# Optimization experiments

Measured on AMD Instinct MI355X. Metric: run time of the kernel, lower is better.

The kernel has to match this reference:

```python
import jax, jax.numpy as jnp
import numpy as np

DIM = 512
L = 64            # block_size == attn_block_size (pool=1)
H = 8             # num_heads
HD = DIM // H     # head_dim
KEY = L + 1       # leaf nodes + block node ('64x65' layout)


def setup_inputs() -> dict:
    key = jax.random.key(0)
    ks = jax.random.split(key, 8)
    B, N, C = 2, 32768, DIM
    nb = N // L
    x = jax.random.normal(ks[0], (B, N, C), dtype=jnp.float32)
    attn_mask = jax.random.randint(ks[1], (B, nb, L, KEY), 0, 2, dtype=jnp.int32)
    # ensure the block node is always attendable so no query row is fully masked
    attn_mask = attn_mask.at[:, :, :, L].set(1)
    edge_feats = jax.random.normal(ks[2], (B, nb, L, KEY, 4), dtype=jnp.float32)
    qkv_w = jax.random.normal(ks[3], (3 * C, C), dtype=jnp.float32) * 0.02
    qkv_b = jax.random.normal(ks[4], (3 * C,), dtype=jnp.float32) * 0.02
    proj_w = jax.random.normal(ks[5], (C, C), dtype=jnp.float32) * 0.02
    proj_b = jax.random.normal(ks[6], (C,), dtype=jnp.float32) * 0.02
    eg_w = jax.random.normal(ks[7], (H, 4), dtype=jnp.float32) * 0.01
    eg_b = jnp.zeros((H,), dtype=jnp.float32)
    return {"x": x, "attn_mask": attn_mask, "edge_feats": edge_feats,
            "qkv_w": qkv_w, "qkv_b": qkv_b, "proj_w": proj_w, "proj_b": proj_b,
            "eg_w": eg_w, "eg_b": eg_b}


def reference(x, attn_mask, edge_feats, qkv_w, qkv_b, proj_w, proj_b, eg_w, eg_b):
    B, N, C = x.shape
    nb = N // L
    scale = HD ** -0.5

    xb = x.reshape(B, nb, L, C)                         # queries = leaf nodes
    block_node = xb.mean(axis=2, keepdims=True)         # [B, nb, 1, C]
    kv = jnp.concatenate([xb, block_node], axis=2)      # [B, nb, KEY, C]

    q = xb @ qkv_w[:C].T + qkv_b[:C]
    k = kv @ qkv_w[C:2 * C].T + qkv_b[C:2 * C]
    v = kv @ qkv_w[2 * C:].T + qkv_b[2 * C:]

    q = q.reshape(B, nb, L, H, HD)
    k = k.reshape(B, nb, KEY, H, HD)
    v = v.reshape(B, nb, KEY, H, HD)

    scores = jnp.einsum('bnqhd,bnkhd->bnqkh', q, k) * scale

    # physics bias: zero special (block) node + diagonal, channel 3 forced to 1
    bias = edge_feats[..., :4]
    bias = bias.at[:, :, :, L, :].set(0.0).at[:, :, :, L, 3].set(1.0)
    idx = jnp.arange(L)
    bias = bias.at[:, :, idx, idx, :].set(0.0).at[:, :, idx, idx, 3].set(1.0)

    scores = scores + bias[..., 3:4]

    masked = (attn_mask == 0)[..., None]                # [B, nb, q, k, 1]
    scores = jnp.where(masked, -jnp.inf, scores)
    attn_probs = jax.nn.softmax(scores, axis=3)

    lew = bias @ eg_w.T + eg_b                          # [B, nb, q, k, H]
    lew = jnp.where(masked, 0.0, lew)
    combined = attn_probs + lew

    out = jnp.einsum('bnqkh,bnkhd->bnqhd', combined, v).reshape(B, nb, L, C)
    out = out @ proj_w.T + proj_b
    return out.reshape(B, N, C)
```

## Files before the change

### kernel.cpp

```cpp
#include <hip/hip_runtime.h>
#include <hip/hip_bf16.h>
#include <math.h>

constexpr int LQ   = 64;
constexpr int KEYS = 65;
constexpr int NH   = 8;
constexpr int DH   = 64;
constexpr int CC   = 512;
constexpr int TOK  = 65536;
constexpr int NBLK = 1024;
constexpr int MEXT = TOK + NBLK;
constexpr int QKVLD = 3 * CC;

using s16x8 = __attribute__((ext_vector_type(8))) short;
using f32x4 = __attribute__((ext_vector_type(4))) float;

__device__ __forceinline__ unsigned short f2bf(float f) {
  unsigned int u = __float_as_uint(f);
  u += 0x7fffu + ((u >> 16) & 1u);
  return (unsigned short)(u >> 16);
}

__global__ __launch_bounds__(256) void prep_x_kernel(const float* __restrict__ x,
                                                     unsigned short* __restrict__ xe) {
  const int blk = blockIdx.x;
  const int c = threadIdx.x * 2;
  const long base = (long)blk * LQ * CC;
  float s0 = 0.f, s1 = 0.f;
  for (int r = 0; r < LQ; ++r) {
    const float2 v = *(const float2*)(x + base + (long)r * CC + c);
    s0 += v.x; s1 += v.y;
    unsigned int p = (unsigned int)f2bf(v.x) | ((unsigned int)f2bf(v.y) << 16);
    *(unsigned int*)(xe + base + (long)r * CC + c) = p;
  }
  unsigned int pm = (unsigned int)f2bf(s0 * (1.f / 64.f)) |
                    ((unsigned int)f2bf(s1 * (1.f / 64.f)) << 16);
  *(unsigned int*)(xe + ((long)TOK + blk) * CC + c) = pm;
}

__global__ __launch_bounds__(256) void prep_w_kernel(const float* __restrict__ qkvw,
                                                     const float* __restrict__ projw,
                                                     unsigned short* __restrict__ wq,
                                                     unsigned short* __restrict__ wp) {
  const int i = blockIdx.x * 256 + threadIdx.x;
  const float* src; unsigned short* dst; int j;
  if (i < 196608) { src = qkvw; dst = wq; j = i; }
  else            { src = projw; dst = wp; j = i - 196608; }
  const float4 v = *(const float4*)(src + (long)j * 4);
  unsigned int lo = (unsigned int)f2bf(v.x) | ((unsigned int)f2bf(v.y) << 16);
  unsigned int hi = (unsigned int)f2bf(v.z) | ((unsigned int)f2bf(v.w) << 16);
  uint2 o; o.x = lo; o.y = hi;
  *(uint2*)(dst + (long)j * 4) = o;
}

template <bool OUT_F32>
__global__ __launch_bounds__(256) void gemm_bt_kernel(
    const unsigned short* __restrict__ A,
    const unsigned short* __restrict__ Bw,
    const float* __restrict__ bias,
    void* __restrict__ Cv,
    int M, int Nn, int K, int tilesN) {
  __shared__ unsigned short lA[128 * 32];
  __shared__ unsigned short lB[128 * 32];
  const int bm = blockIdx.x / tilesN;
  const int bn = blockIdx.x % tilesN;
  const int t = threadIdx.x;
  const int w = t >> 6, lane = t & 63;
  const int l15 = lane & 15, l4 = lane >> 4;
  const int wr = w >> 1, wc = w & 1;
  const int srow = lane >> 2;
  const int scol = (lane & 3) * 8;
  const long rowA0 = (long)bm * 128;
  const long rowB0 = (long)bn * 128;
  f32x4 acc[4][4] = {};
  for (int kk = 0; kk < K; kk += 32) {
#pragma unroll
    for (int i = 0; i < 2; ++i) {
      const int rc = w + 4 * i;
      const unsigned short* gA = A + (rowA0 + rc * 16 + srow) * K + kk + scol;
      const unsigned short* gB = Bw + (rowB0 + rc * 16 + srow) * K + kk + scol;
      __builtin_amdgcn_global_load_lds((const __attribute__((address_space(1))) void*)gA,
                                       (__attribute__((address_space(3))) void*)(lA + rc * 16 * 32),
                                       16, 0, 0);
      __builtin_amdgcn_global_load_lds((const __attribute__((address_space(1))) void*)gB,
                                       (__attribute__((address_space(3))) void*)(lB + rc * 16 * 32),
                                       16, 0, 0);
    }
    __syncthreads();
    s16x8 af[4], bfr[4];
#pragma unroll
    for (int m = 0; m < 4; ++m)
      af[m] = *(const s16x8*)(lA + (wr * 64 + m * 16 + l15) * 32 + l4 * 8);
#pragma unroll
    for (int n = 0; n < 4; ++n)
      bfr[n] = *(const s16x8*)(lB + (wc * 64 + n * 16 + l15) * 32 + l4 * 8);
#pragma unroll
    for (int m = 0; m < 4; ++m)
#pragma unroll
      for (int n = 0; n < 4; ++n)
        acc[m][n] = __builtin_amdgcn_mfma_f32_16x16x32_bf16(af[m], bfr[n], acc[m][n], 0, 0, 0);
    __syncthreads();
  }
#pragma unroll
  for (int m = 0; m < 4; ++m) {
    const long row0 = rowA0 + wr * 64 + m * 16 + l4 * 4;
#pragma unroll
    for (int n = 0; n < 4; ++n) {
      const int col = (int)rowB0 + wc * 64 + n * 16 + l15;
      const float bv = bias[col];
#pragma unroll
      for (int r = 0; r < 4; ++r) {
        const float v = acc[m][n][r] + bv;
        if (OUT_F32) ((float*)Cv)[(row0 + r) * (long)Nn + col] = v;
        else ((unsigned short*)Cv)[(row0 + r) * (long)Nn + col] = f2bf(v);
      }
    }
  }
}

__global__ __launch_bounds__(512) void attn_kernel(
    const unsigned short* __restrict__ QKV,
    const int* __restrict__ amask,
    const float* __restrict__ edge,
    const float* __restrict__ egw,
    const float* __restrict__ egb,
    unsigned short* __restrict__ AO) {
  __shared__ unsigned short PS[NH][16 * 104];
  const int blk = blockIdx.x;
  const int t = threadIdx.x;
  const int h = t >> 6, lane = t & 63;
  const int l15 = lane & 15, l4 = lane >> 4;
  const long tokb = (long)blk * LQ;
  const long bnrow = (long)TOK + blk;
  const unsigned short* Qb = QKV + h * DH;
  const unsigned short* Kb = QKV + CC + h * DH;
  const unsigned short* Vb = QKV + 2 * CC + h * DH;
  const float eg0 = egw[h * 4 + 0], eg1 = egw[h * 4 + 1];
  const float eg2 = egw[h * 4 + 2], eg3 = egw[h * 4 + 3];
  const float egB = egb[h];
  unsigned short* myP = &PS[h][0];

  s16x8 vb[3][4];
#pragma unroll
  for (int dt = 0; dt < 4; ++dt) {
#pragma unroll
    for (int ks = 0; ks < 2; ++ks) {
      s16x8 f;
#pragma unroll
      for (int j = 0; j < 8; ++j) {
        const int key = ks * 32 + l4 * 8 + j;
        f[j] = (short)Vb[(tokb + key) * QKVLD + dt * 16 + l15];
      }
      vb[ks][dt] = f;
    }
    s16x8 f2 = {0, 0, 0, 0, 0, 0, 0, 0};
    if (l4 == 0) f2[0] = (short)Vb[bnrow * QKVLD + dt * 16 + l15];
    vb[2][dt] = f2;
  }

  for (int i = 0; i < 4; ++i) {
    const s16x8 aq0 = *(const s16x8*)(Qb + (tokb + i * 16 + l15) * QKVLD + l4 * 8);
    const s16x8 aq1 = *(const s16x8*)(Qb + (tokb + i * 16 + l15) * QKVLD + 32 + l4 * 8);
    f32x4 sc[5];
#pragma unroll
    for (int jc = 0; jc < 5; ++jc) sc[jc] = {0.f, 0.f, 0.f, 0.f};
#pragma unroll
    for (int jc = 0; jc < 4; ++jc) {
      const s16x8 kf0 = *(const s16x8*)(Kb + (tokb + jc * 16 + l15) * QKVLD + l4 * 8);
      const s16x8 kf1 = *(const s16x8*)(Kb + (tokb + jc * 16 + l15) * QKVLD + 32 + l4 * 8);
      sc[jc] = __builtin_amdgcn_mfma_f32_16x16x32_bf16(aq0, kf0, sc[jc], 0, 0, 0);
      sc[jc] = __builtin_amdgcn_mfma_f32_16x16x32_bf16(aq1, kf1, sc[jc], 0, 0, 0);
    }
    {
      s16x8 kf0 = {0, 0, 0, 0, 0, 0, 0, 0};
      s16x8 kf1 = {0, 0, 0, 0, 0, 0, 0, 0};
      if (l15 == 0) {
        kf0 = *(const s16x8*)(Kb + bnrow * QKVLD + l4 * 8);
        kf1 = *(const s16x8*)(Kb + bnrow * QKVLD + 32 + l4 * 8);
      }
      sc[4] = __builtin_amdgcn_mfma_f32_16x16x32_bf16(aq0, kf0, sc[4], 0, 0, 0);
      sc[4] = __builtin_amdgcn_mfma_f32_16x16x32_bf16(aq1, kf1, sc[4], 0, 0, 0);
    }

    float sv[5][4], lw[5][4];
#pragma unroll
    for (int jc = 0; jc < 5; ++jc) {
      const int k = jc * 16 + l15;
#pragma unroll
      for (int r = 0; r < 4; ++r) {
        const int qq = i * 16 + l4 * 4 + r;
        float val = sc[jc][r] * 0.125f;
        float lv = 0.f;
        if (k <= 64) {
          const long eidx = (tokb + qq) * KEYS + k;
          const int m = amask[eidx];
          float ex, ey, ez, ew;
          if (k == 64 || k == qq) { ex = 0.f; ey = 0.f; ez = 0.f; ew = 1.f; }
          else {
            const float4 e = *(const float4*)(edge + eidx * 4);
            ex = e.x; ey = e.y; ez = e.z; ew = e.w;
          }
          if (m != 0) {
            val += ew;
            lv = ex * eg0 + ey * eg1 + ez * eg2 + ew * eg3 + egB;
          } else val = -INFINITY;
        } else val = -INFINITY;
        sv[jc][r] = val; lw[jc][r] = lv;
      }
    }

#pragma unroll
    for (int r = 0; r < 4; ++r) {
      float mx = sv[0][r];
#pragma unroll
      for (int jc = 1; jc < 5; ++jc) mx = fmaxf(mx, sv[jc][r]);
      mx = fmaxf(mx, __shfl_xor(mx, 1));
      mx = fmaxf(mx, __shfl_xor(mx, 2));
      mx = fmaxf(mx, __shfl_xor(mx, 4));
      mx = fmaxf(mx, __shfl_xor(mx, 8));
      float p[5], sum = 0.f;
#pragma unroll
      for (int jc = 0; jc < 5; ++jc) { p[jc] = __expf(sv[jc][r] - mx); sum += p[jc]; }
      sum += __shfl_xor(sum, 1);
      sum += __shfl_xor(sum, 2);
      sum += __shfl_xor(sum, 4);
      sum += __shfl_xor(sum, 8);
      const float inv = 1.f / sum;
      const int qrow = l4 * 4 + r;
#pragma unroll
      for (int jc = 0; jc < 5; ++jc)
        myP[qrow * 104 + jc * 16 + l15] = f2bf(p[jc] * inv + lw[jc][r]);
      myP[qrow * 104 + 80 + l15] = 0;
    }
    __syncthreads();

    const s16x8 pa0 = *(const s16x8*)(myP + l15 * 104 + l4 * 8);
    const s16x8 pa1 = *(const s16x8*)(myP + l15 * 104 + 32 + l4 * 8);
    const s16x8 pa2 = *(const s16x8*)(myP + l15 * 104 + 64 + l4 * 8);
#pragma unroll
    for (int dt = 0; dt < 4; ++dt) {
      f32x4 oa = {0.f, 0.f, 0.f, 0.f};
      oa = __builtin_amdgcn_mfma_f32_16x16x32_bf16(pa0, vb[0][dt], oa, 0, 0, 0);
      oa = __builtin_amdgcn_mfma_f32_16x16x32_bf16(pa1, vb[1][dt], oa, 0, 0, 0);
      oa = __builtin_amdgcn_mfma_f32_16x16x32_bf16(pa2, vb[2][dt], oa, 0, 0, 0);
#pragma unroll
      for (int r = 0; r < 4; ++r)
        AO[(tokb + i * 16 + l4 * 4 + r) * (long)CC + h * DH + dt * 16 + l15] = f2bf(oa[r]);
    }
    __syncthreads();
  }
}

extern "C" void kernel_launch(void* const* d_in, const int* in_sizes, int n_in,
                              void* d_out, int out_size, void* d_ws, size_t ws_size,
                              hipStream_t stream) {
  const float* x = (const float*)d_in[0];
  const int* amask = (const int*)d_in[1];
  const float* edge = (const float*)d_in[2];
  const float* qkvw = (const float*)d_in[3];
  const float* qkvb = (const float*)d_in[4];
  const float* projw = (const float*)d_in[5];
  const float* projb = (const float*)d_in[6];
  const float* egw = (const float*)d_in[7];
  const float* egb = (const float*)d_in[8];

  char* ws = (char*)d_ws;
  unsigned short* xe  = (unsigned short*)ws;
  unsigned short* qkv = (unsigned short*)(ws + (size_t)68157440);
  unsigned short* wq  = (unsigned short*)(ws + (size_t)272629760);
  unsigned short* wp  = (unsigned short*)(ws + (size_t)274202624);
  unsigned short* ao  = xe;

  prep_x_kernel<<<dim3(NBLK), dim3(256), 0, stream>>>(x, xe);
  prep_w_kernel<<<dim3(1024), dim3(256), 0, stream>>>(qkvw, projw, wq, wp);
  gemm_bt_kernel<false><<<dim3(520 * 12), dim3(256), 0, stream>>>(
      xe, wq, qkvb, (void*)qkv, MEXT, 1536, 512, 12);
  attn_kernel<<<dim3(NBLK), dim3(512), 0, stream>>>(qkv, amask, edge, egw, egb, ao);
  gemm_bt_kernel<true><<<dim3(512 * 4), dim3(256), 0, stream>>>(
      ao, wp, projb, d_out, TOK, 512, 512, 4);
}
```

Baseline: 745.3 us.

## Swizzle GEMM LDS, transpose V output, coalesce attention loads and stores

The QKV GEMM now uses a 64-wide K step with an XOR-swizzled shared-memory layout and block-index swizzling. Its epilogue writes Q/K through LDS for coalesced vector stores and writes V transposed into a separate buffer. The attention kernel reads V with vector loads instead of scalar gathers and hoists the K fragments out of the query loop. It also removes the block barriers, since each wave owns its own LDS slice, and stages the output through LDS for coalesced stores. The transposed V writes are strided, and dropping the barriers relies on wave-local LDS ordering.

```diff
diff --git a/kernel.cpp b/kernel.cpp
--- a/kernel.cpp
+++ b/kernel.cpp
@@ -10,7 +10,6 @@
 constexpr int TOK  = 65536;
 constexpr int NBLK = 1024;
 constexpr int MEXT = TOK + NBLK;
-constexpr int QKVLD = 3 * CC;
 
 using s16x8 = __attribute__((ext_vector_type(8))) short;
 using f32x4 = __attribute__((ext_vector_type(4))) float;
@@ -53,73 +52,116 @@
   *(uint2*)(dst + (long)j * 4) = o;
 }
 
-template <bool OUT_F32>
+template <int MODE>
 __global__ __launch_bounds__(256) void gemm_bt_kernel(
     const unsigned short* __restrict__ A,
     const unsigned short* __restrict__ Bw,
     const float* __restrict__ bias,
-    void* __restrict__ Cv,
-    int M, int Nn, int K, int tilesN) {
-  __shared__ unsigned short lA[128 * 32];
-  __shared__ unsigned short lB[128 * 32];
-  const int bm = blockIdx.x / tilesN;
-  const int bn = blockIdx.x % tilesN;
+    void* __restrict__ out0,
+    unsigned short* __restrict__ out1,
+    int M, int Nn, int K, int tilesN, int cpx) {
+  __shared__ unsigned short sm[16384];
+  const int bid = blockIdx.x;
+  const int swz = (bid & 7) * cpx + (bid >> 3);
+  const int bm = swz / tilesN, bn = swz % tilesN;
   const int t = threadIdx.x;
   const int w = t >> 6, lane = t & 63;
   const int l15 = lane & 15, l4 = lane >> 4;
   const int wr = w >> 1, wc = w & 1;
-  const int srow = lane >> 2;
-  const int scol = (lane & 3) * 8;
+  const int lrow = lane >> 3;
+  const int lcol = ((lane & 7) ^ lrow) << 3;
+  const int fsw = l15 & 7;
   const long rowA0 = (long)bm * 128;
-  const long rowB0 = (long)bn * 128;
+  const int rowB0 = bn * 128;
   f32x4 acc[4][4] = {};
-  for (int kk = 0; kk < K; kk += 32) {
-#pragma unroll
-    for (int i = 0; i < 2; ++i) {
-      const int rc = w + 4 * i;
-      const unsigned short* gA = A + (rowA0 + rc * 16 + srow) * K + kk + scol;
-      const unsigned short* gB = Bw + (rowB0 + rc * 16 + srow) * K + kk + scol;
+  for (int kk = 0; kk < K; kk += 64) {
+#pragma unroll
+    for (int c = 0; c < 4; ++c) {
+      const int rr = c * 32 + w * 8 + lrow;
+      const unsigned short* gA = A + (rowA0 + rr) * K + kk + lcol;
+      const unsigned short* gB = Bw + (long)(rowB0 + rr) * K + kk + lcol;
       __builtin_amdgcn_global_load_lds((const __attribute__((address_space(1))) void*)gA,
-                                       (__attribute__((address_space(3))) void*)(lA + rc * 16 * 32),
+                                       (__attribute__((address_space(3))) void*)(sm + c * 2048 + w * 512),
                                        16, 0, 0);
       __builtin_amdgcn_global_load_lds((const __attribute__((address_space(1))) void*)gB,
-                                       (__attribute__((address_space(3))) void*)(lB + rc * 16 * 32),
+                                       (__attribute__((address_space(3))) void*)(sm + 8192 + c * 2048 + w * 512),
                                        16, 0, 0);
     }
     __syncthreads();
-    s16x8 af[4], bfr[4];
+    s16x8 af[2][4], bf[2][4];
+#pragma unroll
+    for (int ks = 0; ks < 2; ++ks) {
+#pragma unroll
+      for (int m = 0; m < 4; ++m)
+        af[ks][m] = *(const s16x8*)(sm + (wr * 64 + m * 16 + l15) * 64 + (((ks * 4 + l4) ^ fsw) << 3));
+#pragma unroll
+      for (int n = 0; n < 4; ++n)
+        bf[ks][n] = *(const s16x8*)(sm + 8192 + (wc * 64 + n * 16 + l15) * 64 + (((ks * 4 + l4) ^ fsw) << 3));
+    }
+#pragma unroll
+    for (int ks = 0; ks < 2; ++ks)
+#pragma unroll
+      for (int m = 0; m < 4; ++m)
+#pragma unroll
+        for (int n = 0; n < 4; ++n)
+          acc[m][n] = __builtin_amdgcn_mfma_f32_16x16x32_bf16(af[ks][m], bf[ks][n], acc[m][n], 0, 0, 0);
+    __syncthreads();
+  }
+
+  if (MODE == 1) {
+    float* C = (float*)out0;
+#pragma unroll
+    for (int m = 0; m < 4; ++m) {
+      const long row0 = rowA0 + wr * 64 + m * 16 + l4 * 4;
+#pragma unroll
+      for (int n = 0; n < 4; ++n) {
+        const int col = rowB0 + wc * 64 + n * 16 + l15;
+        const float bv = bias[col];
+#pragma unroll
+        for (int r = 0; r < 4; ++r)
+          C[(row0 + r) * (long)Nn + col] = acc[m][n][r] + bv;
+      }
+    }
+  } else if (rowB0 < 1024) {
 #pragma unroll
     for (int m = 0; m < 4; ++m)
-      af[m] = *(const s16x8*)(lA + (wr * 64 + m * 16 + l15) * 32 + l4 * 8);
-#pragma unroll
-    for (int n = 0; n < 4; ++n)
-      bfr[n] = *(const s16x8*)(lB + (wc * 64 + n * 16 + l15) * 32 + l4 * 8);
+#pragma unroll
+      for (int n = 0; n < 4; ++n) {
+        const int col = wc * 64 + n * 16 + l15;
+        const float bv = bias[rowB0 + col];
+#pragma unroll
+        for (int r = 0; r < 4; ++r) {
+          const int row = wr * 64 + m * 16 + l4 * 4 + r;
+          sm[row * 128 + (((col >> 3) ^ (row & 7)) << 3) + (col & 7)] = f2bf(acc[m][n][r] + bv);
+        }
+      }
+    __syncthreads();
+    unsigned short* qk = (unsigned short*)out0;
+#pragma unroll
+    for (int j = 0; j < 8; ++j) {
+      const int idx = j * 256 + t;
+      const int row = idx >> 4, g = idx & 15;
+      const s16x8 v = *(const s16x8*)(sm + row * 128 + ((g ^ (row & 7)) << 3));
+      *(s16x8*)(qk + (rowA0 + row) * 1024 + rowB0 + g * 8) = v;
+    }
+  } else {
 #pragma unroll
     for (int m = 0; m < 4; ++m)
 #pragma unroll
-      for (int n = 0; n < 4; ++n)
-        acc[m][n] = __builtin_amdgcn_mfma_f32_16x16x32_bf16(af[m], bfr[n], acc[m][n], 0, 0, 0);
-    __syncthreads();
-  }
-#pragma unroll
-  for (int m = 0; m < 4; ++m) {
-    const long row0 = rowA0 + wr * 64 + m * 16 + l4 * 4;
-#pragma unroll
-    for (int n = 0; n < 4; ++n) {
-      const int col = (int)rowB0 + wc * 64 + n * 16 + l15;
-      const float bv = bias[col];
-#pragma unroll
-      for (int r = 0; r < 4; ++r) {
-        const float v = acc[m][n][r] + bv;
-        if (OUT_F32) ((float*)Cv)[(row0 + r) * (long)Nn + col] = v;
-        else ((unsigned short*)Cv)[(row0 + r) * (long)Nn + col] = f2bf(v);
+      for (int n = 0; n < 4; ++n) {
+        const int colg = rowB0 + wc * 64 + n * 16 + l15;
+        const float bv = bias[colg];
+        uint2 o;
+        o.x = (unsigned)f2bf(acc[m][n][0] + bv) | ((unsigned)f2bf(acc[m][n][1] + bv) << 16);
+        o.y = (unsigned)f2bf(acc[m][n][2] + bv) | ((unsigned)f2bf(acc[m][n][3] + bv) << 16);
+        *(uint2*)(out1 + (long)(colg - 1024) * MEXT + rowA0 + wr * 64 + m * 16 + l4 * 4) = o;
       }
-    }
   }
 }
 
 __global__ __launch_bounds__(512) void attn_kernel(
-    const unsigned short* __restrict__ QKV,
+    const unsigned short* __restrict__ QK,
+    const unsigned short* __restrict__ VT,
     const int* __restrict__ amask,
     const float* __restrict__ edge,
     const float* __restrict__ egw,
@@ -132,63 +174,58 @@
   const int l15 = lane & 15, l4 = lane >> 4;
   const long tokb = (long)blk * LQ;
   const long bnrow = (long)TOK + blk;
-  const unsigned short* Qb = QKV + h * DH;
-  const unsigned short* Kb = QKV + CC + h * DH;
-  const unsigned short* Vb = QKV + 2 * CC + h * DH;
+  const unsigned short* Qb = QK + h * DH;
+  const unsigned short* Kb = QK + CC + h * DH;
+  const unsigned short* Vt = VT + (long)h * DH * MEXT;
   const float eg0 = egw[h * 4 + 0], eg1 = egw[h * 4 + 1];
   const float eg2 = egw[h * 4 + 2], eg3 = egw[h * 4 + 3];
   const float egB = egb[h];
   unsigned short* myP = &PS[h][0];
 
+  s16x8 kf[4][2];
+#pragma unroll
+  for (int jc = 0; jc < 4; ++jc) {
+    kf[jc][0] = *(const s16x8*)(Kb + (tokb + jc * 16 + l15) * 1024 + l4 * 8);
+    kf[jc][1] = *(const s16x8*)(Kb + (tokb + jc * 16 + l15) * 1024 + 32 + l4 * 8);
+  }
+  s16x8 kf4[2] = {{0,0,0,0,0,0,0,0},{0,0,0,0,0,0,0,0}};
+  if (l15 == 0) {
+    kf4[0] = *(const s16x8*)(Kb + bnrow * 1024 + l4 * 8);
+    kf4[1] = *(const s16x8*)(Kb + bnrow * 1024 + 32 + l4 * 8);
+  }
+
   s16x8 vb[3][4];
 #pragma unroll
   for (int dt = 0; dt < 4; ++dt) {
-#pragma unroll
-    for (int ks = 0; ks < 2; ++ks) {
-      s16x8 f;
-#pragma unroll
-      for (int j = 0; j < 8; ++j) {
-        const int key = ks * 32 + l4 * 8 + j;
-        f[j] = (short)Vb[(tokb + key) * QKVLD + dt * 16 + l15];
-      }
-      vb[ks][dt] = f;
-    }
+    const unsigned short* vrow = Vt + (long)(dt * 16 + l15) * MEXT;
+    vb[0][dt] = *(const s16x8*)(vrow + tokb + l4 * 8);
+    vb[1][dt] = *(const s16x8*)(vrow + tokb + 32 + l4 * 8);
     s16x8 f2 = {0, 0, 0, 0, 0, 0, 0, 0};
-    if (l4 == 0) f2[0] = (short)Vb[bnrow * QKVLD + dt * 16 + l15];
+    if (l4 == 0) f2[0] = (short)vrow[bnrow];
     vb[2][dt] = f2;
   }
 
   for (int i = 0; i < 4; ++i) {
-    const s16x8 aq0 = *(const s16x8*)(Qb + (tokb + i * 16 + l15) * QKVLD + l4 * 8);
-    const s16x8 aq1 = *(const s16x8*)(Qb + (tokb + i * 16 + l15) * QKVLD + 32 + l4 * 8);
+    const s16x8 aq0 = *(const s16x8*)(Qb + (tokb + i * 16 + l15) * 1024 + l4 * 8);
+    const s16x8 aq1 = *(const s16x8*)(Qb + (tokb + i * 16 + l15) * 1024 + 32 + l4 * 8);
     f32x4 sc[5];
 #pragma unroll
     for (int jc = 0; jc < 5; ++jc) sc[jc] = {0.f, 0.f, 0.f, 0.f};
 #pragma unroll
     for (int jc = 0; jc < 4; ++jc) {
-      const s16x8 kf0 = *(const s16x8*)(Kb + (tokb + jc * 16 + l15) * QKVLD + l4 * 8);
-      const s16x8 kf1 = *(const s16x8*)(Kb + (tokb + jc * 16 + l15) * QKVLD + 32 + l4 * 8);
-      sc[jc] = __builtin_amdgcn_mfma_f32_16x16x32_bf16(aq0, kf0, sc[jc], 0, 0, 0);
-      sc[jc] = __builtin_amdgcn_mfma_f32_16x16x32_bf16(aq1, kf1, sc[jc], 0, 0, 0);
-    }
-    {
-      s16x8 kf0 = {0, 0, 0, 0, 0, 0, 0, 0};
-      s16x8 kf1 = {0, 0, 0, 0, 0, 0, 0, 0};
-      if (l15 == 0) {
-        kf0 = *(const s16x8*)(Kb + bnrow * QKVLD + l4 * 8);
-        kf1 = *(const s16x8*)(Kb + bnrow * QKVLD + 32 + l4 * 8);
-      }
-      sc[4] = __builtin_amdgcn_mfma_f32_16x16x32_bf16(aq0, kf0, sc[4], 0, 0, 0);
-      sc[4] = __builtin_amdgcn_mfma_f32_16x16x32_bf16(aq1, kf1, sc[4], 0, 0, 0);
-    }
-
-    float sv[5][4], lw[5][4];
-#pragma unroll
-    for (int jc = 0; jc < 5; ++jc) {
-      const int k = jc * 16 + l15;
-#pragma unroll
-      for (int r = 0; r < 4; ++r) {
-        const int qq = i * 16 + l4 * 4 + r;
+      sc[jc] = __builtin_amdgcn_mfma_f32_16x16x32_bf16(aq0, kf[jc][0], sc[jc], 0, 0, 0);
+      sc[jc] = __builtin_amdgcn_mfma_f32_16x16x32_bf16(aq1, kf[jc][1], sc[jc], 0, 0, 0);
+    }
+    sc[4] = __builtin_amdgcn_mfma_f32_16x16x32_bf16(aq0, kf4[0], sc[4], 0, 0, 0);
+    sc[4] = __builtin_amdgcn_mfma_f32_16x16x32_bf16(aq1, kf4[1], sc[4], 0, 0, 0);
+
+#pragma unroll
+    for (int r = 0; r < 4; ++r) {
+      const int qq = i * 16 + l4 * 4 + r;
+      float sv[5], lw[5];
+#pragma unroll
+      for (int jc = 0; jc < 5; ++jc) {
+        const int k = jc * 16 + l15;
         float val = sc[jc][r] * 0.125f;
         float lv = 0.f;
         if (k <= 64) {
@@ -205,22 +242,16 @@
             lv = ex * eg0 + ey * eg1 + ez * eg2 + ew * eg3 + egB;
           } else val = -INFINITY;
         } else val = -INFINITY;
-        sv[jc][r] = val; lw[jc][r] = lv;
+        sv[jc] = val; lw[jc] = lv;
       }
-    }
-
-#pragma unroll
-    for (int r = 0; r < 4; ++r) {
-      float mx = sv[0][r];
-#pragma unroll
-      for (int jc = 1; jc < 5; ++jc) mx = fmaxf(mx, sv[jc][r]);
+      float mx = fmaxf(fmaxf(fmaxf(sv[0], sv[1]), fmaxf(sv[2], sv[3])), sv[4]);
       mx = fmaxf(mx, __shfl_xor(mx, 1));
       mx = fmaxf(mx, __shfl_xor(mx, 2));
       mx = fmaxf(mx, __shfl_xor(mx, 4));
       mx = fmaxf(mx, __shfl_xor(mx, 8));
       float p[5], sum = 0.f;
 #pragma unroll
-      for (int jc = 0; jc < 5; ++jc) { p[jc] = __expf(sv[jc][r] - mx); sum += p[jc]; }
+      for (int jc = 0; jc < 5; ++jc) { p[jc] = __expf(sv[jc] - mx); sum += p[jc]; }
       sum += __shfl_xor(sum, 1);
       sum += __shfl_xor(sum, 2);
       sum += __shfl_xor(sum, 4);
@@ -229,10 +260,9 @@
       const int qrow = l4 * 4 + r;
 #pragma unroll
       for (int jc = 0; jc < 5; ++jc)
-        myP[qrow * 104 + jc * 16 + l15] = f2bf(p[jc] * inv + lw[jc][r]);
+        myP[qrow * 104 + jc * 16 + l15] = f2bf(p[jc] * inv + lw[jc]);
       myP[qrow * 104 + 80 + l15] = 0;
     }
-    __syncthreads();
 
     const s16x8 pa0 = *(const s16x8*)(myP + l15 * 104 + l4 * 8);
     const s16x8 pa1 = *(const s16x8*)(myP + l15 * 104 + 32 + l4 * 8);
@@ -245,9 +275,16 @@
       oa = __builtin_amdgcn_mfma_f32_16x16x32_bf16(pa2, vb[2][dt], oa, 0, 0, 0);
 #pragma unroll
       for (int r = 0; r < 4; ++r)
-        AO[(tokb + i * 16 + l4 * 4 + r) * (long)CC + h * DH + dt * 16 + l15] = f2bf(oa[r]);
-    }
-    __syncthreads();
+        myP[(l4 * 4 + r) * 104 + dt * 16 + l15] = f2bf(oa[r]);
+    }
+    {
+      const int row16 = lane >> 2, gsel = lane & 3;
+      const s16x8 o0 = *(const s16x8*)(myP + row16 * 104 + gsel * 8);
+      const s16x8 o1 = *(const s16x8*)(myP + row16 * 104 + (gsel + 4) * 8);
+      unsigned short* dst = AO + (tokb + i * 16 + row16) * CC + h * DH;
+      *(s16x8*)(dst + gsel * 8) = o0;
+      *(s16x8*)(dst + (gsel + 4) * 8) = o1;
+    }
   }
 }
 
@@ -265,17 +302,18 @@
   const float* egb = (const float*)d_in[8];
 
   char* ws = (char*)d_ws;
-  unsigned short* xe  = (unsigned short*)ws;
-  unsigned short* qkv = (unsigned short*)(ws + (size_t)68157440);
-  unsigned short* wq  = (unsigned short*)(ws + (size_t)272629760);
-  unsigned short* wp  = (unsigned short*)(ws + (size_t)274202624);
-  unsigned short* ao  = xe;
+  unsigned short* xe = (unsigned short*)ws;
+  unsigned short* qk = (unsigned short*)(ws + (size_t)68157440);
+  unsigned short* vt = (unsigned short*)(ws + (size_t)204472320);
+  unsigned short* wq = (unsigned short*)(ws + (size_t)272629760);
+  unsigned short* wp = (unsigned short*)(ws + (size_t)274202624);
+  unsigned short* ao = xe;
 
   prep_x_kernel<<<dim3(NBLK), dim3(256), 0, stream>>>(x, xe);
   prep_w_kernel<<<dim3(1024), dim3(256), 0, stream>>>(qkvw, projw, wq, wp);
-  gemm_bt_kernel<false><<<dim3(520 * 12), dim3(256), 0, stream>>>(
-      xe, wq, qkvb, (void*)qkv, MEXT, 1536, 512, 12);
-  attn_kernel<<<dim3(NBLK), dim3(512), 0, stream>>>(qkv, amask, edge, egw, egb, ao);
-  gemm_bt_kernel<true><<<dim3(512 * 4), dim3(256), 0, stream>>>(
-      ao, wp, projb, d_out, TOK, 512, 512, 4);
-}
+  gemm_bt_kernel<0><<<dim3(520 * 12), dim3(256), 0, stream>>>(
+      xe, wq, qkvb, (void*)qk, vt, MEXT, 1536, 512, 12, 780);
+  attn_kernel<<<dim3(NBLK), dim3(512), 0, stream>>>(qk, vt, amask, edge, egw, egb, ao);
+  gemm_bt_kernel<1><<<dim3(512 * 4), dim3(256), 0, stream>>>(
+      ao, wp, projb, d_out, nullptr, TOK, 512, 512, 4, 256);
+}
```

Measured after the change: 733.9 us. Within noise of the previous version (-1.5%).
